# Kernel optimization log

Hardware: AMD Instinct MI355X
Metric: run time of the kernel (lower is better)

## Reference

```python
import jax, jax.numpy as jnp
import numpy as np

HEAD_SIZE = 64


def setup_inputs() -> dict:
    key = jax.random.key(0)
    ks = jax.random.split(key, 8)
    B, S, W, H = 16, 2048, 768, HEAD_SIZE
    inp = jax.random.normal(ks[0], (B, S, W), dtype=jnp.float32)
    # key-padding mask, broadcastable to [B, S, S]; ensure at least one valid key per row
    mask = jax.random.randint(ks[1], (B, 1, S), 0, 2, dtype=jnp.int32)
    mask = mask.at[:, :, 0].set(1)
    scale = 1.0 / np.sqrt(W)
    Wq = jax.random.normal(ks[2], (W, H), dtype=jnp.float32) * scale
    bq = jax.random.normal(ks[3], (H,), dtype=jnp.float32) * 0.02
    Wk = jax.random.normal(ks[4], (W, H), dtype=jnp.float32) * scale
    bk = jax.random.normal(ks[5], (H,), dtype=jnp.float32) * 0.02
    Wv = jax.random.normal(ks[6], (W, H), dtype=jnp.float32) * scale
    bv = jax.random.normal(ks[7], (H,), dtype=jnp.float32) * 0.02
    return {"input": inp, "mask": mask, "Wq": Wq, "bq": bq, "Wk": Wk, "bk": bk, "Wv": Wv, "bv": bv}


def reference(input, mask, Wq, bq, Wk, bk, Wv, bv):
    # Q/K/V projections: [B, S, H]
    Q = input @ Wq + bq
    K = input @ Wk + bk
    V = input @ Wv + bv
    # scores: [B, S, S], scaled by sqrt(head_size)
    scores = jnp.einsum("bqh,bkh->bqk", Q, K) / jnp.sqrt(jnp.float32(HEAD_SIZE))
    scores = jnp.where(mask == 0, -jnp.inf, scores)
    attn = jax.nn.softmax(scores, axis=-1)
    return jnp.einsum("bqk,bkh->bqh", attn, V)
```

## Files before the change

kernel.cpp:

```cpp
#include <hip/hip_runtime.h>

typedef short bf16x8 __attribute__((ext_vector_type(8)));
typedef float f32x4 __attribute__((ext_vector_type(4)));
typedef float f32x16 __attribute__((ext_vector_type(16)));
typedef unsigned int u32x4 __attribute__((ext_vector_type(4)));
typedef unsigned short u16;
typedef unsigned int u32;

#define DEVI static __device__ __forceinline__

#define NB 16
#define NS 2048
#define NW 768
#define NH 64

DEVI u16 f2bf(float x) {
  u32 u = __builtin_bit_cast(u32, x);
  u += 0x7fffu + ((u >> 16) & 1u);
  return (u16)(u >> 16);
}

DEVI u32 cvtpk(float lo, float hi) {
  u32 r;
  asm("v_cvt_pk_bf16_f32 %0, %1, %2" : "=v"(r) : "v"(lo), "v"(hi));
  return r;
}

DEVI f32x4 mfma16(bf16x8 a, bf16x8 b, f32x4 c) {
  return __builtin_amdgcn_mfma_f32_16x16x32_bf16(a, b, c, 0, 0, 0);
}
DEVI f32x16 mfma32(bf16x8 a, bf16x8 b, f32x16 c) {
  return __builtin_amdgcn_mfma_f32_32x32x16_bf16(a, b, c, 0, 0, 0);
}

DEVI int swz(int row, int col) { return ((row * 64 + col) * 2) ^ ((row & 7) << 4); }


__global__ __launch_bounds__(256) void prep_weights(
    const float* __restrict__ Wq, const float* __restrict__ Wk,
    const float* __restrict__ Wv, u16* __restrict__ wsW) {
  int tid = blockIdx.x * 256 + threadIdx.x;
  int tile = tid >> 6, lane = tid & 63;
  int p = tile / 96, rem = tile % 96;
  int nct = rem / 24, kch = rem % 24;
  const float* Wsrc = (p == 0) ? Wq : ((p == 1) ? Wk : Wv);
  int k0 = kch * 32 + (lane >> 4) * 8;
  int n = nct * 16 + (lane & 15);
  u16 h[8];
#pragma unroll
  for (int i = 0; i < 8; i++) h[i] = f2bf(Wsrc[(k0 + i) * NH + n]);
  uint4 v;
  v.x = (u32)h[0] | ((u32)h[1] << 16);
  v.y = (u32)h[2] | ((u32)h[3] << 16);
  v.z = (u32)h[4] | ((u32)h[5] << 16);
  v.w = (u32)h[6] | ((u32)h[7] << 16);
  ((uint4*)wsW)[tile * 64 + lane] = v;
}

__global__ __launch_bounds__(256) void prep_bias(const int* __restrict__ mask,
                                                 float* __restrict__ biasF) {
  int i = blockIdx.x * 256 + threadIdx.x;
  biasF[i] = mask[i] ? 0.0f : -1.0e5f;
}

__global__ __launch_bounds__(256) void qkv_proj(
    const float* __restrict__ inp, const u16* __restrict__ wsW,
    const float* __restrict__ bq, const float* __restrict__ bk,
    const float* __restrict__ bv, u16* __restrict__ Qf, u16* __restrict__ Kf,
    u16* __restrict__ Vf) {
  __shared__ __align__(16) u16 A_lds[32 * 64];
  int tid = threadIdx.x;
  int w = tid >> 6, lane = tid & 63, g = lane >> 4, l15 = lane & 15;
  int row0 = blockIdx.x * 32;

  f32x4 acc[2][3];
#pragma unroll
  for (int rt = 0; rt < 2; rt++)
#pragma unroll
    for (int ct = 0; ct < 3; ct++) acc[rt][ct] = (f32x4)0.0f;

  int sr = tid >> 4, sc4 = (tid & 15) * 4;
  int sr1 = (tid + 256) >> 4;

  float4 a_reg[2];
  bf16x8 w_reg[3][2];
  a_reg[0] = *(const float4*)(inp + (size_t)(row0 + sr) * NW + sc4);
  a_reg[1] = *(const float4*)(inp + (size_t)(row0 + sr1) * NW + sc4);
#pragma unroll
  for (int ct = 0; ct < 3; ct++)
#pragma unroll
    for (int kk = 0; kk < 2; kk++)
      w_reg[ct][kk] =
          *(const bf16x8*)(wsW + (size_t)((w * 3 + ct) * 24 + kk) * 512 + lane * 8);

  for (int chunk = 0; chunk < 12; chunk++) {
    __syncthreads();
    {
      float4 v = a_reg[0];
      ushort4 h4;
      h4.x = f2bf(v.x); h4.y = f2bf(v.y); h4.z = f2bf(v.z); h4.w = f2bf(v.w);
      *(ushort4*)((char*)A_lds + swz(sr, sc4)) = h4;
      v = a_reg[1];
      h4.x = f2bf(v.x); h4.y = f2bf(v.y); h4.z = f2bf(v.z); h4.w = f2bf(v.w);
      *(ushort4*)((char*)A_lds + swz(sr1, sc4)) = h4;
    }
    int cn = (chunk < 11) ? chunk + 1 : 11;
    float4 a_nxt[2];
    bf16x8 w_nxt[3][2];
    a_nxt[0] = *(const float4*)(inp + (size_t)(row0 + sr) * NW + cn * 64 + sc4);
    a_nxt[1] = *(const float4*)(inp + (size_t)(row0 + sr1) * NW + cn * 64 + sc4);
#pragma unroll
    for (int ct = 0; ct < 3; ct++)
#pragma unroll
      for (int kk = 0; kk < 2; kk++)
        w_nxt[ct][kk] = *(const bf16x8*)(
            wsW + (size_t)((w * 3 + ct) * 24 + cn * 2 + kk) * 512 + lane * 8);
    __syncthreads();
    bf16x8 af[2][2];
#pragma unroll
    for (int rt = 0; rt < 2; rt++)
#pragma unroll
      for (int kk = 0; kk < 2; kk++)
        af[rt][kk] = *(const bf16x8*)((const char*)A_lds +
                                      swz(rt * 16 + l15, kk * 32 + g * 8));
#pragma unroll
    for (int ct = 0; ct < 3; ct++)
#pragma unroll
      for (int kk = 0; kk < 2; kk++) {
        acc[0][ct] = mfma16(af[0][kk], w_reg[ct][kk], acc[0][ct]);
        acc[1][ct] = mfma16(af[1][kk], w_reg[ct][kk], acc[1][ct]);
      }
    a_reg[0] = a_nxt[0];
    a_reg[1] = a_nxt[1];
#pragma unroll
    for (int ct = 0; ct < 3; ct++)
#pragma unroll
      for (int kk = 0; kk < 2; kk++) w_reg[ct][kk] = w_nxt[ct][kk];
  }

  int b = row0 >> 11;
  size_t bT = (size_t)b * 64 + ((row0 & 2047) >> 5);
#pragma unroll
  for (int ct = 0; ct < 3; ct++) {
    int gct = w * 3 + ct;
    int p3 = gct >> 2;
    int n = (gct & 3) * 16 + l15;
    const float* bias = (p3 == 0) ? bq : ((p3 == 1) ? bk : bv);
    float bbv = bias[n];
    if (p3 < 2) {
      u16* base = (p3 == 0) ? Qf : Kf;
      int kk = gct & 3;
      int hin = (l15 >> 3) & 1, j = l15 & 7;
#pragma unroll
      for (int rt = 0; rt < 2; rt++)
#pragma unroll
        for (int reg = 0; reg < 4; reg++)
          base[((bT * 4 + kk) * 64 + hin * 32 + rt * 16 + g * 4 + reg) * 8 + j] =
              f2bf(acc[rt][ct][reg] + bbv);
    } else {
      int ht = n >> 5, lanev = ((g >> 1) & 1) * 32 + (n & 31), jb = (g & 1) * 4;
#pragma unroll
      for (int rt = 0; rt < 2; rt++) {
        uint2 pp;
        pp.x = (u32)f2bf(acc[rt][ct][0] + bbv) |
               ((u32)f2bf(acc[rt][ct][1] + bbv) << 16);
        pp.y = (u32)f2bf(acc[rt][ct][2] + bbv) |
               ((u32)f2bf(acc[rt][ct][3] + bbv) << 16);
        *(uint2*)(Vf + (((bT * 2 + rt) * 2 + ht) * 64 + lanev) * 8 + jb) = pp;
      }
    }
  }
}

__global__ __launch_bounds__(256) void attn(
    const u16* __restrict__ Qf, const u16* __restrict__ Kf,
    const u16* __restrict__ Vf, const float* __restrict__ biasF,
    float* __restrict__ out) {
  __shared__ __align__(16) char smem[34304];
  int tid = threadIdx.x;
  int w = tid >> 6, lane = tid & 63;
  int l31 = lane & 31, hi = lane >> 5;
  int bid = blockIdx.x;
  int b = (bid & 7) * 2 + ((bid >> 3) & 1);
  int q0t = bid >> 4;
  const float* bb = biasF + (size_t)b * NS;
  float* corrL = (float*)smem + w * 32;

  const float SC = 0.18033688011112043f;

  size_t bQT = (size_t)b * 64 + q0t;
  bf16x8 qf[4];
#pragma unroll
  for (int kk = 0; kk < 4; kk++)
    qf[kk] = *(const bf16x8*)(Qf + (bQT * 4 + kk) * 512 + lane * 8);

  f32x16 acc[2];
  acc[0] = (f32x16)0.0f;
  acc[1] = (f32x16)0.0f;
  float m_run = -1.0e4f, l_run = 0.0f;

  size_t tbase = (size_t)b * 64 + w * 16;
  bf16x8 kf[4];
#pragma unroll
  for (int kk = 0; kk < 4; kk++)
    kf[kk] = *(const bf16x8*)(Kf + (tbase * 4 + kk) * 512 + lane * 8);

  for (int t = 0; t < 16; t++) {
    int kv0 = w * 512 + t * 32;
    size_t bKT = tbase + t;
    size_t bKN = tbase + ((t < 15) ? t + 1 : t);
    bf16x8 kn[4];
#pragma unroll
    for (int kk = 0; kk < 4; kk++)
      kn[kk] = *(const bf16x8*)(Kf + (bKN * 4 + kk) * 512 + lane * 8);
    bf16x8 vf[2][2];
#pragma unroll
    for (int ht = 0; ht < 2; ht++)
#pragma unroll
      for (int ks = 0; ks < 2; ks++)
        vf[ht][ks] = *(const bf16x8*)(Vf + ((bKT * 2 + ks) * 2 + ht) * 512 +
                                      lane * 8);
    float4 b4[4];
#pragma unroll
    for (int m = 0; m < 4; m++)
      b4[m] = *(const float4*)(bb + kv0 + m * 8 + hi * 4);

    f32x16 sT = (f32x16)0.0f;
#pragma unroll
    for (int kk = 0; kk < 4; kk++) sT = mfma32(kf[kk], qf[kk], sT);

    float tm = -1.0e30f;
#pragma unroll
    for (int r = 0; r < 16; r++) {
      sT[r] = fmaf(sT[r], SC, b4[r >> 2][r & 3]);
      tm = fmaxf(tm, sT[r]);
    }
    tm = fmaxf(tm, __shfl_xor(tm, 32));

    if (!__all(tm <= m_run + 8.0f)) {
      float mn = fmaxf(m_run, tm);
      float corr = exp2f(m_run - mn);
      m_run = mn;
      l_run *= corr;
      if (hi == 0) corrL[l31] = corr;
      float4 c4[4];
#pragma unroll
      for (int m = 0; m < 4; m++)
        c4[m] = *(const float4*)(corrL + m * 8 + hi * 4);
#pragma unroll
      for (int r = 0; r < 16; r++) {
        float cq = c4[r >> 2][r & 3];
        acc[0][r] *= cq;
        acc[1][r] *= cq;
      }
    }

    float p[16];
    float rs = 0.0f;
#pragma unroll
    for (int r = 0; r < 16; r++) {
      p[r] = exp2f(sT[r] - m_run);
      rs += p[r];
    }
    rs += __shfl_xor(rs, 32);
    l_run += rs;

    u32 c[8];
#pragma unroll
    for (int i = 0; i < 8; i++) c[i] = cvtpk(p[2 * i], p[2 * i + 1]);
    u32 x[8];
#pragma unroll
    for (int i = 0; i < 8; i++) x[i] = (u32)__shfl_xor((int)c[i], 32);
    u32x4 w0, w1;
    w0.x = hi ? x[2] : c[0];
    w0.y = hi ? x[3] : c[1];
    w0.z = hi ? c[2] : x[0];
    w0.w = hi ? c[3] : x[1];
    w1.x = hi ? x[6] : c[4];
    w1.y = hi ? x[7] : c[5];
    w1.z = hi ? c[6] : x[4];
    w1.w = hi ? c[7] : x[5];
    bf16x8 pa0 = __builtin_bit_cast(bf16x8, w0);
    bf16x8 pa1 = __builtin_bit_cast(bf16x8, w1);

    acc[0] = mfma32(pa0, vf[0][0], acc[0]);
    acc[1] = mfma32(pa0, vf[1][0], acc[1]);
    acc[0] = mfma32(pa1, vf[0][1], acc[0]);
    acc[1] = mfma32(pa1, vf[1][1], acc[1]);

#pragma unroll
    for (int kk = 0; kk < 4; kk++) kf[kk] = kn[kk];
  }

  __syncthreads();
  float* accL = (float*)smem;
  float* mlL = (float*)(smem + 33280);
#pragma unroll
  for (int ht = 0; ht < 2; ht++)
#pragma unroll
    for (int r = 0; r < 16; r++) {
      int q = (r & 3) + 8 * (r >> 2) + 4 * hi;
      accL[(w * 32 + q) * 65 + ht * 32 + l31] = acc[ht][r];
    }
  if (hi == 0) {
    mlL[(w * 32 + l31) * 2 + 0] = m_run;
    mlL[(w * 32 + l31) * 2 + 1] = l_run;
  }
  __syncthreads();

#pragma unroll
  for (int i = 0; i < 8; i++) {
    int idx = tid + i * 256;
    int row = idx >> 6, h = idx & 63;
    float m[4], l[4];
#pragma unroll
    for (int z = 0; z < 4; z++) {
      m[z] = mlL[(z * 32 + row) * 2 + 0];
      l[z] = mlL[(z * 32 + row) * 2 + 1];
    }
    float M = fmaxf(fmaxf(m[0], m[1]), fmaxf(m[2], m[3]));
    float den = 0.0f, o = 0.0f;
#pragma unroll
    for (int z = 0; z < 4; z++) {
      float e = exp2f(m[z] - M);
      den += e * l[z];
      o += e * accL[(z * 32 + row) * 65 + h];
    }
    out[((size_t)b * NS + q0t * 32 + row) * NH + h] = o / den;
  }
}

extern "C" void kernel_launch(void* const* d_in, const int* in_sizes, int n_in,
                              void* d_out, int out_size, void* d_ws,
                              size_t ws_size, hipStream_t stream) {
  const float* inp = (const float*)d_in[0];
  const int* mask = (const int*)d_in[1];
  const float* Wq = (const float*)d_in[2];
  const float* bq = (const float*)d_in[3];
  const float* Wk = (const float*)d_in[4];
  const float* bk = (const float*)d_in[5];
  const float* Wv = (const float*)d_in[6];
  const float* bv = (const float*)d_in[7];
  float* out = (float*)d_out;

  char* ws = (char*)d_ws;
  u16* wsW = (u16*)ws;
  u16* wsQf = (u16*)(ws + (1u << 20));
  u16* wsKf = (u16*)(ws + (1u << 20) + (4u << 20));
  u16* wsVf = (u16*)(ws + (1u << 20) + (8u << 20));
  float* wsBias = (float*)(ws + (13u << 20));

  prep_weights<<<dim3(72), dim3(256), 0, stream>>>(Wq, Wk, Wv, wsW);
  prep_bias<<<dim3(NB * NS / 256), dim3(256), 0, stream>>>(mask, wsBias);
  qkv_proj<<<dim3((NB * NS) / 32), dim3(256), 0, stream>>>(inp, wsW, bq, bk,
                                                           bv, wsQf, wsKf, wsVf);
  attn<<<dim3(NB * NS / 32), dim3(256), 0, stream>>>(wsQf, wsKf, wsVf, wsBias,
                                                     out);
}
```

Before: 75.29 us.

## Load projection inputs directly to registers and double attention block query tiles

```diff
diff --git a/kernel.cpp b/kernel.cpp
--- a/kernel.cpp
+++ b/kernel.cpp
@@ -26,14 +26,21 @@
   return r;
 }
 
+DEVI bf16x8 cvt8(float4 a, float4 b) {
+  u32x4 r;
+  r.x = cvtpk(a.x, a.y);
+  r.y = cvtpk(a.z, a.w);
+  r.z = cvtpk(b.x, b.y);
+  r.w = cvtpk(b.z, b.w);
+  return __builtin_bit_cast(bf16x8, r);
+}
+
 DEVI f32x4 mfma16(bf16x8 a, bf16x8 b, f32x4 c) {
   return __builtin_amdgcn_mfma_f32_16x16x32_bf16(a, b, c, 0, 0, 0);
 }
 DEVI f32x16 mfma32(bf16x8 a, bf16x8 b, f32x16 c) {
   return __builtin_amdgcn_mfma_f32_32x32x16_bf16(a, b, c, 0, 0, 0);
 }
-
-DEVI int swz(int row, int col) { return ((row * 64 + col) * 2) ^ ((row & 7) << 4); }
 
 
 __global__ __launch_bounds__(256) void prep_weights(
@@ -68,7 +75,6 @@
     const float* __restrict__ bq, const float* __restrict__ bk,
     const float* __restrict__ bv, u16* __restrict__ Qf, u16* __restrict__ Kf,
     u16* __restrict__ Vf) {
-  __shared__ __align__(16) u16 A_lds[32 * 64];
   int tid = threadIdx.x;
   int w = tid >> 6, lane = tid & 63, g = lane >> 4, l15 = lane & 15;
   int row0 = blockIdx.x * 32;
@@ -79,63 +85,38 @@
 #pragma unroll
     for (int ct = 0; ct < 3; ct++) acc[rt][ct] = (f32x4)0.0f;
 
-  int sr = tid >> 4, sc4 = (tid & 15) * 4;
-  int sr1 = (tid + 256) >> 4;
-
-  float4 a_reg[2];
-  bf16x8 w_reg[3][2];
-  a_reg[0] = *(const float4*)(inp + (size_t)(row0 + sr) * NW + sc4);
-  a_reg[1] = *(const float4*)(inp + (size_t)(row0 + sr1) * NW + sc4);
-#pragma unroll
-  for (int ct = 0; ct < 3; ct++)
-#pragma unroll
-    for (int kk = 0; kk < 2; kk++)
-      w_reg[ct][kk] =
-          *(const bf16x8*)(wsW + (size_t)((w * 3 + ct) * 24 + kk) * 512 + lane * 8);
-
+#pragma unroll 2
   for (int chunk = 0; chunk < 12; chunk++) {
-    __syncthreads();
-    {
-      float4 v = a_reg[0];
-      ushort4 h4;
-      h4.x = f2bf(v.x); h4.y = f2bf(v.y); h4.z = f2bf(v.z); h4.w = f2bf(v.w);
-      *(ushort4*)((char*)A_lds + swz(sr, sc4)) = h4;
-      v = a_reg[1];
-      h4.x = f2bf(v.x); h4.y = f2bf(v.y); h4.z = f2bf(v.z); h4.w = f2bf(v.w);
-      *(ushort4*)((char*)A_lds + swz(sr1, sc4)) = h4;
-    }
-    int cn = (chunk < 11) ? chunk + 1 : 11;
-    float4 a_nxt[2];
-    bf16x8 w_nxt[3][2];
-    a_nxt[0] = *(const float4*)(inp + (size_t)(row0 + sr) * NW + cn * 64 + sc4);
-    a_nxt[1] = *(const float4*)(inp + (size_t)(row0 + sr1) * NW + cn * 64 + sc4);
+    const float* cb = inp + (size_t)row0 * NW + chunk * 64;
+    float4 a[2][2][2];
+#pragma unroll
+    for (int rt = 0; rt < 2; rt++)
+#pragma unroll
+      for (int kk = 0; kk < 2; kk++) {
+        const float* p = cb + (size_t)(rt * 16 + l15) * NW + kk * 32 + g * 8;
+        a[rt][kk][0] = *(const float4*)p;
+        a[rt][kk][1] = *(const float4*)(p + 4);
+      }
+    bf16x8 wr[3][2];
 #pragma unroll
     for (int ct = 0; ct < 3; ct++)
 #pragma unroll
       for (int kk = 0; kk < 2; kk++)
-        w_nxt[ct][kk] = *(const bf16x8*)(
-            wsW + (size_t)((w * 3 + ct) * 24 + cn * 2 + kk) * 512 + lane * 8);
-    __syncthreads();
+        wr[ct][kk] = *(const bf16x8*)(
+            wsW + (size_t)((w * 3 + ct) * 24 + chunk * 2 + kk) * 512 + lane * 8);
     bf16x8 af[2][2];
 #pragma unroll
     for (int rt = 0; rt < 2; rt++)
 #pragma unroll
       for (int kk = 0; kk < 2; kk++)
-        af[rt][kk] = *(const bf16x8*)((const char*)A_lds +
-                                      swz(rt * 16 + l15, kk * 32 + g * 8));
+        af[rt][kk] = cvt8(a[rt][kk][0], a[rt][kk][1]);
 #pragma unroll
     for (int ct = 0; ct < 3; ct++)
 #pragma unroll
       for (int kk = 0; kk < 2; kk++) {
-        acc[0][ct] = mfma16(af[0][kk], w_reg[ct][kk], acc[0][ct]);
-        acc[1][ct] = mfma16(af[1][kk], w_reg[ct][kk], acc[1][ct]);
+        acc[0][ct] = mfma16(af[0][kk], wr[ct][kk], acc[0][ct]);
+        acc[1][ct] = mfma16(af[1][kk], wr[ct][kk], acc[1][ct]);
       }
-    a_reg[0] = a_nxt[0];
-    a_reg[1] = a_nxt[1];
-#pragma unroll
-    for (int ct = 0; ct < 3; ct++)
-#pragma unroll
-      for (int kk = 0; kk < 2; kk++) w_reg[ct][kk] = w_nxt[ct][kk];
   }
 
   int b = row0 >> 11;
@@ -172,23 +153,24 @@
   }
 }
 
-__global__ __launch_bounds__(256) void attn(
+__global__ __launch_bounds__(512) void attn(
     const u16* __restrict__ Qf, const u16* __restrict__ Kf,
     const u16* __restrict__ Vf, const float* __restrict__ biasF,
     float* __restrict__ out) {
-  __shared__ __align__(16) char smem[34304];
+  __shared__ __align__(16) char smem[68608];
   int tid = threadIdx.x;
   int w = tid >> 6, lane = tid & 63;
   int l31 = lane & 31, hi = lane >> 5;
+  int qt = w >> 2, kc = w & 3;
   int bid = blockIdx.x;
   int b = (bid & 7) * 2 + ((bid >> 3) & 1);
-  int q0t = bid >> 4;
+  int qp = bid >> 4;
   const float* bb = biasF + (size_t)b * NS;
   float* corrL = (float*)smem + w * 32;
 
   const float SC = 0.18033688011112043f;
 
-  size_t bQT = (size_t)b * 64 + q0t;
+  size_t bQT = (size_t)b * 64 + qp * 2 + qt;
   bf16x8 qf[4];
 #pragma unroll
   for (int kk = 0; kk < 4; kk++)
@@ -199,14 +181,14 @@
   acc[1] = (f32x16)0.0f;
   float m_run = -1.0e4f, l_run = 0.0f;
 
-  size_t tbase = (size_t)b * 64 + w * 16;
+  size_t tbase = (size_t)b * 64 + kc * 16;
   bf16x8 kf[4];
 #pragma unroll
   for (int kk = 0; kk < 4; kk++)
     kf[kk] = *(const bf16x8*)(Kf + (tbase * 4 + kk) * 512 + lane * 8);
 
   for (int t = 0; t < 16; t++) {
-    int kv0 = w * 512 + t * 32;
+    int kv0 = kc * 512 + t * 32;
     size_t bKT = tbase + t;
     size_t bKN = tbase + ((t < 15) ? t + 1 : t);
     bf16x8 kn[4];
@@ -226,15 +208,18 @@
       b4[m] = *(const float4*)(bb + kv0 + m * 8 + hi * 4);
 
     f32x16 sT = (f32x16)0.0f;
+    __builtin_amdgcn_s_setprio(1);
 #pragma unroll
     for (int kk = 0; kk < 4; kk++) sT = mfma32(kf[kk], qf[kk], sT);
-
-    float tm = -1.0e30f;
-#pragma unroll
-    for (int r = 0; r < 16; r++) {
-      sT[r] = fmaf(sT[r], SC, b4[r >> 2][r & 3]);
-      tm = fmaxf(tm, sT[r]);
-    }
+    __builtin_amdgcn_s_setprio(0);
+
+#pragma unroll
+    for (int r = 0; r < 16; r++) sT[r] = fmaf(sT[r], SC, b4[r >> 2][r & 3]);
+    float tm0 = fmaxf(fmaxf(sT[0], sT[1]), fmaxf(sT[2], sT[3]));
+    float tm1 = fmaxf(fmaxf(sT[4], sT[5]), fmaxf(sT[6], sT[7]));
+    float tm2 = fmaxf(fmaxf(sT[8], sT[9]), fmaxf(sT[10], sT[11]));
+    float tm3 = fmaxf(fmaxf(sT[12], sT[13]), fmaxf(sT[14], sT[15]));
+    float tm = fmaxf(fmaxf(tm0, tm1), fmaxf(tm2, tm3));
     tm = fmaxf(tm, __shfl_xor(tm, 32));
 
     if (!__all(tm <= m_run + 8.0f)) {
@@ -256,37 +241,35 @@
     }
 
     float p[16];
-    float rs = 0.0f;
-#pragma unroll
-    for (int r = 0; r < 16; r++) {
-      p[r] = exp2f(sT[r] - m_run);
-      rs += p[r];
-    }
+#pragma unroll
+    for (int r = 0; r < 16; r++) p[r] = exp2f(sT[r] - m_run);
+    float rs0 = (p[0] + p[1]) + (p[2] + p[3]);
+    float rs1 = (p[4] + p[5]) + (p[6] + p[7]);
+    float rs2 = (p[8] + p[9]) + (p[10] + p[11]);
+    float rs3 = (p[12] + p[13]) + (p[14] + p[15]);
+    float rs = (rs0 + rs1) + (rs2 + rs3);
     rs += __shfl_xor(rs, 32);
     l_run += rs;
 
     u32 c[8];
 #pragma unroll
     for (int i = 0; i < 8; i++) c[i] = cvtpk(p[2 * i], p[2 * i + 1]);
-    u32 x[8];
-#pragma unroll
-    for (int i = 0; i < 8; i++) x[i] = (u32)__shfl_xor((int)c[i], 32);
+    asm volatile("v_permlane32_swap_b32 %0, %1" : "+v"(c[0]), "+v"(c[2]));
+    asm volatile("v_permlane32_swap_b32 %0, %1" : "+v"(c[1]), "+v"(c[3]));
+    asm volatile("v_permlane32_swap_b32 %0, %1" : "+v"(c[4]), "+v"(c[6]));
+    asm volatile("v_permlane32_swap_b32 %0, %1" : "+v"(c[5]), "+v"(c[7]));
     u32x4 w0, w1;
-    w0.x = hi ? x[2] : c[0];
-    w0.y = hi ? x[3] : c[1];
-    w0.z = hi ? c[2] : x[0];
-    w0.w = hi ? c[3] : x[1];
-    w1.x = hi ? x[6] : c[4];
-    w1.y = hi ? x[7] : c[5];
-    w1.z = hi ? c[6] : x[4];
-    w1.w = hi ? c[7] : x[5];
+    w0.x = c[0]; w0.y = c[1]; w0.z = c[2]; w0.w = c[3];
+    w1.x = c[4]; w1.y = c[5]; w1.z = c[6]; w1.w = c[7];
     bf16x8 pa0 = __builtin_bit_cast(bf16x8, w0);
     bf16x8 pa1 = __builtin_bit_cast(bf16x8, w1);
 
+    __builtin_amdgcn_s_setprio(1);
     acc[0] = mfma32(pa0, vf[0][0], acc[0]);
     acc[1] = mfma32(pa0, vf[1][0], acc[1]);
     acc[0] = mfma32(pa1, vf[0][1], acc[0]);
     acc[1] = mfma32(pa1, vf[1][1], acc[1]);
+    __builtin_amdgcn_s_setprio(0);
 
 #pragma unroll
     for (int kk = 0; kk < 4; kk++) kf[kk] = kn[kk];
@@ -294,29 +277,29 @@
 
   __syncthreads();
   float* accL = (float*)smem;
-  float* mlL = (float*)(smem + 33280);
+  float* mlL = (float*)(smem + 66560);
 #pragma unroll
   for (int ht = 0; ht < 2; ht++)
 #pragma unroll
     for (int r = 0; r < 16; r++) {
       int q = (r & 3) + 8 * (r >> 2) + 4 * hi;
-      accL[(w * 32 + q) * 65 + ht * 32 + l31] = acc[ht][r];
+      accL[(kc * 64 + qt * 32 + q) * 65 + ht * 32 + l31] = acc[ht][r];
     }
   if (hi == 0) {
-    mlL[(w * 32 + l31) * 2 + 0] = m_run;
-    mlL[(w * 32 + l31) * 2 + 1] = l_run;
+    mlL[(kc * 64 + qt * 32 + l31) * 2 + 0] = m_run;
+    mlL[(kc * 64 + qt * 32 + l31) * 2 + 1] = l_run;
   }
   __syncthreads();
 
 #pragma unroll
   for (int i = 0; i < 8; i++) {
-    int idx = tid + i * 256;
+    int idx = tid + i * 512;
     int row = idx >> 6, h = idx & 63;
     float m[4], l[4];
 #pragma unroll
     for (int z = 0; z < 4; z++) {
-      m[z] = mlL[(z * 32 + row) * 2 + 0];
-      l[z] = mlL[(z * 32 + row) * 2 + 1];
+      m[z] = mlL[(z * 64 + row) * 2 + 0];
+      l[z] = mlL[(z * 64 + row) * 2 + 1];
     }
     float M = fmaxf(fmaxf(m[0], m[1]), fmaxf(m[2], m[3]));
     float den = 0.0f, o = 0.0f;
@@ -324,9 +307,9 @@
     for (int z = 0; z < 4; z++) {
       float e = exp2f(m[z] - M);
       den += e * l[z];
-      o += e * accL[(z * 32 + row) * 65 + h];
-    }
-    out[((size_t)b * NS + q0t * 32 + row) * NH + h] = o / den;
+      o += e * accL[(z * 64 + row) * 65 + h];
+    }
+    out[((size_t)b * NS + qp * 64 + row) * NH + h] = o / den;
   }
 }
 
@@ -354,6 +337,6 @@
   prep_bias<<<dim3(NB * NS / 256), dim3(256), 0, stream>>>(mask, wsBias);
   qkv_proj<<<dim3((NB * NS) / 32), dim3(256), 0, stream>>>(inp, wsW, bq, bk,
                                                            bv, wsQf, wsKf, wsVf);
-  attn<<<dim3(NB * NS / 32), dim3(256), 0, stream>>>(wsQf, wsKf, wsVf, wsBias,
+  attn<<<dim3(NB * NS / 64), dim3(512), 0, stream>>>(wsQf, wsKf, wsVf, wsBias,
                                                      out);
 }
```

Result: slower. 107.3 us (+42.5%).
